# Optimization experiments

Measured on AMD Instinct MI355X. Metric: run time of the kernel, lower is better.

Reference implementation:

```python
import jax, jax.numpy as jnp
import numpy as np

N_P = 2048   # personality nodes
N_W = 89     # word nodes (fixed by user_word_adj[:, :89])
N_ALL = N_P + N_W
B = 16384    # users
E2 = 768     # sentence embedding size
UW = 313     # 89 word cols + 224 extra cols -> 32 + 224 = 256 for share1


def setup_inputs() -> dict:
    key = jax.random.key(0)
    ks = jax.random.split(key, 20)
    rn = lambda k, s, sc=0.1: (jax.random.normal(k, s, jnp.float32) * sc)
    pern_adj = jax.random.randint(ks[2], (N_P, N_P), 0, 2, jnp.int32)
    pern_adj = pern_adj.at[jnp.arange(N_P), jnp.arange(N_P)].set(1)
    word_pern_adj = jax.random.randint(ks[3], (N_ALL, N_ALL), 0, 2, jnp.int32)
    word_pern_adj = word_pern_adj.at[jnp.arange(N_ALL), jnp.arange(N_ALL)].set(1)
    return dict(
        pern_feature=rn(ks[0], (N_P, 256), 1.0),
        word_feature=rn(ks[1], (N_W, 256), 1.0),
        pern_adj=pern_adj,
        word_pern_adj=word_pern_adj,
        user_word_adj=jax.random.uniform(ks[4], (B, UW), jnp.float32),
        sentence_embed=rn(ks[5], (B, E2), 1.0),
        w1=rn(ks[6], (8, 256, 32)), a_src1=rn(ks[7], (8, 32)), a_dst1=rn(ks[8], (8, 32)), bias1=jnp.zeros((32,), jnp.float32),
        w2=rn(ks[9], (8, 256, 32)), a_src2=rn(ks[10], (8, 32)), a_dst2=rn(ks[11], (8, 32)), bias2=jnp.zeros((32,), jnp.float32),
        W_s1=rn(ks[12], (256, 128)), b_s1=jnp.zeros((128,), jnp.float32),
        W_s2=rn(ks[13], (E2, 128)), b_s2=jnp.zeros((128,), jnp.float32),
        W_f1=rn(ks[14], (128, 64)), b_f1=jnp.zeros((64,), jnp.float32),
        W_fa=rn(ks[15], (256, 128)), b_fa=jnp.zeros((128,), jnp.float32),
        W_fb=rn(ks[16], (128, 5)), b_fb=jnp.zeros((5,), jnp.float32),
    )


def gat(h, adj, w, a_src, a_dst, bias):
    # h: (n, f_in); w: (H, f_in, f_out); a_src/a_dst: (H, f_out); adj: (n, n) 0/1
    hp = jnp.einsum('nf,hfo->hno', h, w)                      # (H, n, f_out)
    e_src = jnp.einsum('hno,ho->hn', hp, a_src)               # (H, n)
    e_dst = jnp.einsum('hno,ho->hn', hp, a_dst)               # (H, n)
    e = jax.nn.leaky_relu(e_src[:, :, None] + e_dst[:, None, :], 0.2)  # (H, n, n)
    e = jnp.where(adj[None, :, :] > 0, e, jnp.float32(-1e9))
    attn = jax.nn.softmax(e, axis=-1)
    out = jnp.einsum('hnm,hmo->hno', attn, hp) + bias         # (H, n, f_out)
    return out, attn


def reference(pern_feature, word_feature, pern_adj, word_pern_adj,
              user_word_adj, sentence_embed,
              w1, a_src1, a_dst1, bias1, w2, a_src2, a_dst2, bias2,
              W_s1, b_s1, W_s2, b_s2, W_f1, b_f1, W_fa, b_fa, W_fb, b_fb):
    n_p = pern_feature.shape[0]
    # GAT 1 on personality graph
    h1, attn_pp = gat(pern_feature, pern_adj, w1, a_src1, a_dst1, bias1)
    h1 = jax.nn.elu(jnp.transpose(h1, (1, 0, 2)).reshape(n_p, -1))   # (n_p, 256)
    # dropout is identity at eval time
    h1_wp = jnp.concatenate([word_feature, h1], axis=0)               # (n_w+n_p, 256)
    # GAT 2 on word-personality graph, mean over heads
    h2, attn_wp = gat(h1_wp, word_pern_adj, w2, a_src2, a_dst2, bias2)
    h2 = h2.mean(axis=0)                                              # (n_w+n_p, 32)
    h2_word = h2[:word_feature.shape[0], :]                           # (89, 32)
    # user aggregation over word adjacency + row normalization
    x = user_word_adj[:, :N_W] @ h2_word                              # (B, 32)
    x_c = jnp.concatenate([x, user_word_adj[:, N_W:]], axis=1)        # (B, 256)
    x = x_c / x_c.sum(axis=1, keepdims=True)
    # dual heads
    output1 = x @ W_s1 + b_s1
    output2 = sentence_embed @ W_s2 + b_s2
    output1_new = output1 @ W_f1 + b_f1
    output2_new = output2 @ W_f1 + b_f1
    x_temp = jnp.concatenate([output1, output2], axis=1)
    x_temp = jax.nn.relu(x_temp @ W_fa + b_fa) @ W_fb + b_fb
    return (output1_new, output2_new, x_temp, attn_pp, attn_wp, x)
```

## Files before the change

### kernel.cpp

```cpp
#include <hip/hip_runtime.h>
#include <cstdint>
#include <cstddef>

#define N_P 2048
#define N_W 89
#define N_ALLC 2137
#define BQ 16384
#define E2C 768

typedef __attribute__((ext_vector_type(8))) short short8;
typedef __attribute__((ext_vector_type(4))) float float4v;

__device__ __forceinline__ float waveMax(float v){
#pragma unroll
  for (int o = 32; o > 0; o >>= 1) v = fmaxf(v, __shfl_down(v, o, 64));
  return v;
}
__device__ __forceinline__ float waveSum(float v){
#pragma unroll
  for (int o = 32; o > 0; o >>= 1) v += __shfl_down(v, o, 64);
  return v;
}
__device__ __forceinline__ unsigned short f2bf(float f){
  union { float f; unsigned int u; } v; v.f = f;
  unsigned int u = v.u;
  unsigned int r = (u + 0x7FFFu + ((u >> 16) & 1u)) >> 16;
  return (unsigned short)r;
}

__global__ __launch_bounds__(256) void repack_w(const float* __restrict__ w,
                                                float* __restrict__ wrm) {
  int idx = blockIdx.x * 256 + threadIdx.x;
  int f = idx >> 8, c = idx & 255;
  int h = c >> 5, o = c & 31;
  wrm[idx] = w[h * 8192 + f * 32 + o];
}

__global__ __launch_bounds__(256) void repack_wpk(const float* __restrict__ W,
                                                  unsigned short* __restrict__ out,
                                                  int K, int N) {
  int idx = blockIdx.x * 256 + threadIdx.x;
  if (idx >= K * N) return;
  int k = idx / N, n = idx - k * N;
  int kb = k >> 5, q = (k >> 3) & 3, j = k & 7;
  out[((size_t)(kb * 4 + q) * N + n) * 8 + j] = f2bf(W[idx]);
}

__global__ __launch_bounds__(256) void copy_word(const float* __restrict__ wf,
                                                 float* __restrict__ h1wp) {
  int idx = blockIdx.x * 256 + threadIdx.x;
  if (idx < N_W * 256) h1wp[idx] = wf[idx];
}

__global__ __launch_bounds__(256) void gemm_f32(
    const float* __restrict__ A, int lda,
    const float* __restrict__ B, int ldb,
    float* __restrict__ C, int ldc,
    const float* __restrict__ bias,
    int M, int N, int K, int relu)
{
  __shared__ __align__(16) float As[16][68];
  __shared__ __align__(16) float Bs[16][68];
  int t = threadIdx.x;
  int m0 = blockIdx.x * 64, n0 = blockIdx.y * 64;
  int tm = t >> 4, tn = t & 15;
  int ar = t >> 2, ak = (t & 3) * 4;
  int bk = t >> 4, bn = (t & 15) * 4;
  float acc[4][4] = {};
  for (int k0 = 0; k0 < K; k0 += 16) {
    float4 av = {0.f, 0.f, 0.f, 0.f};
    int arow = m0 + ar;
    if (arow < M) av = *(const float4*)(A + (size_t)arow * lda + k0 + ak);
    As[ak][ar] = av.x; As[ak + 1][ar] = av.y; As[ak + 2][ar] = av.z; As[ak + 3][ar] = av.w;
    *(float4*)&Bs[bk][bn] = *(const float4*)(B + (size_t)(k0 + bk) * ldb + n0 + bn);
    __syncthreads();
#pragma unroll
    for (int kk = 0; kk < 16; ++kk) {
      float4 a4 = *(const float4*)&As[kk][tm * 4];
      float4 b4 = *(const float4*)&Bs[kk][tn * 4];
      float a[4] = {a4.x, a4.y, a4.z, a4.w};
      float b[4] = {b4.x, b4.y, b4.z, b4.w};
#pragma unroll
      for (int i = 0; i < 4; ++i)
#pragma unroll
        for (int j = 0; j < 4; ++j) acc[i][j] += a[i] * b[j];
    }
    __syncthreads();
  }
#pragma unroll
  for (int i = 0; i < 4; ++i) {
    int row = m0 + tm * 4 + i;
    if (row < M) {
      float4 v;
      v.x = acc[i][0]; v.y = acc[i][1]; v.z = acc[i][2]; v.w = acc[i][3];
      *(float4*)(C + (size_t)row * ldc + n0 + tn * 4) = v;
    }
  }
}

__global__ __launch_bounds__(256) void gemm_mfma(
    const float* __restrict__ A, int lda,
    const unsigned short* __restrict__ Wpk, int N,
    const float* __restrict__ bias,
    float* __restrict__ C, int ldc,
    int K, int relu)
{
  int t = threadIdx.x;
  int w = t >> 6, lane = t & 63;
  int col = lane & 15, quad = lane >> 4;
  int rowA = blockIdx.x * 64 + w * 16 + col;
  int n0 = blockIdx.y * 64;
  const float* arow = A + (size_t)rowA * lda;
  float4v acc[4];
#pragma unroll
  for (int nt = 0; nt < 4; ++nt) acc[nt] = (float4v){0.f, 0.f, 0.f, 0.f};
  for (int k0 = 0; k0 < K; k0 += 32) {
    const float* ap = arow + k0 + quad * 8;
    float4 f0 = *(const float4*)(ap);
    float4 f1 = *(const float4*)(ap + 4);
    short8 a;
    a[0] = (short)f2bf(f0.x); a[1] = (short)f2bf(f0.y);
    a[2] = (short)f2bf(f0.z); a[3] = (short)f2bf(f0.w);
    a[4] = (short)f2bf(f1.x); a[5] = (short)f2bf(f1.y);
    a[6] = (short)f2bf(f1.z); a[7] = (short)f2bf(f1.w);
    const unsigned short* wb = Wpk + ((size_t)((k0 >> 5) * 4 + quad) * N + n0 + col) * 8;
#pragma unroll
    for (int nt = 0; nt < 4; ++nt) {
      short8 b = *(const short8*)(wb + (size_t)nt * 16 * 8);
      acc[nt] = __builtin_amdgcn_mfma_f32_16x16x32_bf16(a, b, acc[nt], 0, 0, 0);
    }
  }
  int rbase = blockIdx.x * 64 + w * 16 + quad * 4;
#pragma unroll
  for (int nt = 0; nt < 4; ++nt) {
    int c = n0 + nt * 16 + col;
    float bv = bias[c];
#pragma unroll
    for (int r = 0; r < 4; ++r) {
      float v = acc[nt][r] + bv;
      if (relu) v = fmaxf(v, 0.f);
      C[(size_t)(rbase + r) * ldc + c] = v;
    }
  }
}

__global__ __launch_bounds__(256) void esrc_edst(
    const float* __restrict__ hp,
    const float* __restrict__ a_src,
    const float* __restrict__ a_dst,
    float* __restrict__ es, float* __restrict__ ed, int N)
{
  __shared__ float sa[256], sd[256];
  int t = threadIdx.x;
  sa[t] = a_src[t]; sd[t] = a_dst[t];
  __syncthreads();
  int idx = blockIdx.x * 256 + t;
  if (idx >= N * 8) return;
  int n = idx >> 3, h = idx & 7;
  const float* hpp = hp + (size_t)n * 256 + h * 32;
  const float* ap = sa + h * 32;
  const float* dp = sd + h * 32;
  float s = 0.f, d = 0.f;
#pragma unroll
  for (int o = 0; o < 32; ++o) { float v = hpp[o]; s += v * ap[o]; d += v * dp[o]; }
  es[h * N + n] = s; ed[h * N + n] = d;
}

__global__ __launch_bounds__(256) void attn_softmax(
    const float* __restrict__ es, const float* __restrict__ ed,
    const int* __restrict__ adj,
    float* __restrict__ attn,
    int N)
{
  int h = blockIdx.x, n = blockIdx.y;
  int t = threadIdx.x, lane = t & 63, wid = t >> 6;
  __shared__ float red[4];
  float esv = es[h * N + n];
  const float* edh = ed + (size_t)h * N;
  const int* arow = adj + (size_t)n * N;
  float v[9];
  float lmax = -3e38f;
#pragma unroll
  for (int i = 0; i < 9; ++i) {
    int m = i * 256 + t;
    float x = -3e38f;
    if (m < N) {
      float e = esv + edh[m];
      e = (e >= 0.f) ? e : 0.2f * e;
      x = (arow[m] > 0) ? e : -1e9f;
    }
    v[i] = x; lmax = fmaxf(lmax, x);
  }
  lmax = waveMax(lmax);
  if (lane == 0) red[wid] = lmax;
  __syncthreads();
  float gmax = fmaxf(fmaxf(red[0], red[1]), fmaxf(red[2], red[3]));
  __syncthreads();
  float lsum = 0.f;
#pragma unroll
  for (int i = 0; i < 9; ++i) {
    int m = i * 256 + t;
    if (m < N) { float p = __expf(v[i] - gmax); v[i] = p; lsum += p; }
  }
  lsum = waveSum(lsum);
  if (lane == 0) red[wid] = lsum;
  __syncthreads();
  float inv = 1.f / (red[0] + red[1] + red[2] + red[3]);
  float* out = attn + ((size_t)h * N + n) * N;
#pragma unroll
  for (int i = 0; i < 9; ++i) {
    int m = i * 256 + t;
    if (m < N) out[m] = v[i] * inv;
  }
}

__global__ __launch_bounds__(256) void pv1_partial(
    const float* __restrict__ attn,
    const float* __restrict__ hp,
    float* __restrict__ parts)
{
  __shared__ __align__(16) float As[128][68];
  __shared__ __align__(16) float Bs[64][36];
  int t = threadIdx.x;
  int m0 = blockIdx.x * 128;
  int h  = blockIdx.y;
  int ks = blockIdx.z;
  int ro = t >> 3;
  int co = t & 7;
  float acc[4][4] = {};
  const float* abase = attn + ((size_t)h * N_P + m0) * N_P;
  for (int k0 = ks * 512; k0 < ks * 512 + 512; k0 += 64) {
#pragma unroll
    for (int i = 0; i < 8; ++i) {
      int idx = t + i * 256;
      int r = idx >> 4, c4 = idx & 15;
      float4 v = *(const float4*)(abase + (size_t)r * N_P + k0 + c4 * 4);
      *(float4*)&As[r][c4 * 4] = v;
    }
#pragma unroll
    for (int i = 0; i < 2; ++i) {
      int idx = t + i * 256;
      int r = idx >> 3, c4 = idx & 7;
      float4 v = *(const float4*)(hp + (size_t)(k0 + r) * 256 + h * 32 + c4 * 4);
      *(float4*)&Bs[r][c4 * 4] = v;
    }
    __syncthreads();
#pragma unroll 16
    for (int kk = 0; kk < 64; ++kk) {
      float4 b4 = *(const float4*)&Bs[kk][co * 4];
#pragma unroll
      for (int i = 0; i < 4; ++i) {
        float a = As[ro * 4 + i][kk];
        acc[i][0] += a * b4.x; acc[i][1] += a * b4.y;
        acc[i][2] += a * b4.z; acc[i][3] += a * b4.w;
      }
    }
    __syncthreads();
  }
  float* p = parts + (size_t)ks * (N_P * 256);
#pragma unroll
  for (int i = 0; i < 4; ++i) {
    int row = m0 + ro * 4 + i;
    float4 v; v.x = acc[i][0]; v.y = acc[i][1]; v.z = acc[i][2]; v.w = acc[i][3];
    *(float4*)&p[(size_t)row * 256 + h * 32 + co * 4] = v;
  }
}

__global__ __launch_bounds__(256) void pv1_epilogue(
    const float* __restrict__ parts,
    const float* __restrict__ bias,
    float* __restrict__ h1wp)
{
  int idx = blockIdx.x * 256 + threadIdx.x;
  float s = parts[idx] + parts[idx + N_P * 256] + parts[idx + 2 * N_P * 256] + parts[idx + 3 * N_P * 256];
  s += bias[idx & 31];
  h1wp[(size_t)N_W * 256 + idx] = (s > 0.f) ? s : expm1f(s);
}

__global__ __launch_bounds__(256) void h2w_init(const float* __restrict__ bias,
                                                float* __restrict__ h2w) {
  int idx = blockIdx.x * 256 + threadIdx.x;
  if (idx < N_W * 32) h2w[idx] = bias[idx & 31];
}

__global__ __launch_bounds__(256) void pv2(
    const float* __restrict__ attn,
    const float* __restrict__ hp,
    float* __restrict__ h2w)
{
  int n = blockIdx.x, h = blockIdx.y;
  int t = threadIdx.x, g = t >> 5, o = t & 31;
  const float* arow = attn + ((size_t)h * N_ALLC + n) * N_ALLC;
  float acc = 0.f;
  for (int m = g; m < N_ALLC; m += 8) acc += arow[m] * hp[(size_t)m * 256 + h * 32 + o];
  __shared__ float pv[8][33];
  pv[g][o] = acc;
  __syncthreads();
  if (t < 32) {
    float s = 0.f;
#pragma unroll
    for (int gg = 0; gg < 8; ++gg) s += pv[gg][t];
    atomicAdd(&h2w[n * 32 + t], s * 0.125f);
  }
}

__global__ __launch_bounds__(256) void xnorm_kernel(
    const float* __restrict__ uwa,
    const float* __restrict__ h2w,
    float* __restrict__ xout)
{
  __shared__ float urow[4][320];
  __shared__ float xh[4][33];
  __shared__ float inv[4];
  int t = threadIdx.x;
  int b0 = blockIdx.x * 4;
  for (int idx = t; idx < 4 * 313; idx += 256) {
    int r = idx / 313, j = idx - r * 313;
    urow[r][j] = uwa[(size_t)(b0 + r) * 313 + j];
  }
  __syncthreads();
  if (t < 128) {
    int r = t >> 5, o = t & 31;
    float s = 0.f;
    for (int i = 0; i < N_W; ++i) s += urow[r][i] * h2w[i * 32 + o];
    xh[r][o] = s;
  }
  __syncthreads();
  int lane = t & 63, w = t >> 6;
  float ls = 0.f;
  for (int c = lane; c < 256; c += 64) {
    float v = (c < 32) ? xh[w][c] : urow[w][89 + c - 32];
    ls += v;
  }
  ls = waveSum(ls);
  if (lane == 0) inv[w] = 1.f / ls;
  __syncthreads();
  for (int idx = t; idx < 1024; idx += 256) {
    int r = idx >> 8, c = idx & 255;
    float v = (c < 32) ? xh[r][c] : urow[r][89 + c - 32];
    xout[(size_t)(b0 + r) * 256 + c] = v * inv[r];
  }
}

__global__ __launch_bounds__(256) void final5(
    const float* __restrict__ tb,
    const float* __restrict__ Wfb,
    const float* __restrict__ bfb,
    float* __restrict__ out)
{
  __shared__ float tt[32][129];
  __shared__ float wfb[5][128];
  int t = threadIdx.x;
  int b0 = blockIdx.x * 32;
  for (int idx = t; idx < 32 * 128; idx += 256) {
    int r = idx >> 7, c = idx & 127;
    tt[r][c] = tb[(size_t)(b0 + r) * 128 + c];
  }
  for (int idx = t; idx < 640; idx += 256) {
    int q = idx >> 7, j = idx & 127;
    wfb[q][j] = Wfb[j * 5 + q];
  }
  __syncthreads();
  if (t < 160) {
    int q = t >> 5, r = t & 31;
    float s = bfb[q];
    const float* wq = wfb[q];
    for (int j = 0; j < 128; ++j) s += tt[r][j] * wq[j];
    out[(size_t)(b0 + r) * 5 + q] = s;
  }
}

extern "C" void kernel_launch(void* const* d_in, const int* in_sizes, int n_in,
                              void* d_out, int out_size, void* d_ws, size_t ws_size,
                              hipStream_t stream)
{
  const float* pf   = (const float*)d_in[0];
  const float* wf   = (const float*)d_in[1];
  const int*   adj1 = (const int*)d_in[2];
  const int*   adj2 = (const int*)d_in[3];
  const float* uwa  = (const float*)d_in[4];
  const float* sent = (const float*)d_in[5];
  const float* w1   = (const float*)d_in[6];
  const float* as1  = (const float*)d_in[7];
  const float* ad1  = (const float*)d_in[8];
  const float* b1   = (const float*)d_in[9];
  const float* w2   = (const float*)d_in[10];
  const float* as2  = (const float*)d_in[11];
  const float* ad2  = (const float*)d_in[12];
  const float* b2   = (const float*)d_in[13];
  const float* Ws1  = (const float*)d_in[14];
  const float* bs1  = (const float*)d_in[15];
  const float* Ws2  = (const float*)d_in[16];
  const float* bs2  = (const float*)d_in[17];
  const float* Wf1  = (const float*)d_in[18];
  const float* bf1  = (const float*)d_in[19];
  const float* Wfa  = (const float*)d_in[20];
  const float* bfa  = (const float*)d_in[21];
  const float* Wfb  = (const float*)d_in[22];
  const float* bfb  = (const float*)d_in[23];

  float* ws = (float*)d_ws;
  float* wrm1 = ws;
  float* wrm2 = wrm1 + 65536;
  float* hp1  = wrm2 + 65536;
  float* hp2  = hp1 + (size_t)N_P * 256;
  float* es1v = hp2 + (size_t)N_ALLC * 256;
  float* ed1v = es1v + 8 * N_P;
  float* es2v = ed1v + 8 * N_P;
  float* ed2v = es2v + 8 * N_ALLC;
  float* h1wp = ed2v + 8 * N_ALLC;
  float* h2w  = h1wp + (size_t)N_ALLC * 256;
  float* o12  = h2w + N_W * 32;
  float* tbuf = o12 + (size_t)BQ * 256;
  float* parts = tbuf + (size_t)BQ * 128;
  unsigned short* ws1pk = (unsigned short*)(parts + (size_t)4 * N_P * 256);
  unsigned short* ws2pk = ws1pk + 256 * 128;
  unsigned short* wf1pk = ws2pk + 768 * 128;
  unsigned short* wfapk = wf1pk + 128 * 64;

  float* out = (float*)d_out;
  float* out_o1n = out;
  float* out_o2n = out + (size_t)BQ * 64;
  float* out_xt  = out + (size_t)BQ * 128;
  float* out_app = out_xt + (size_t)BQ * 5;
  float* out_awp = out_app + (size_t)8 * N_P * N_P;
  float* out_x   = out_awp + (size_t)8 * N_ALLC * N_ALLC;

  repack_w<<<256, 256, 0, stream>>>(w1, wrm1);
  repack_w<<<256, 256, 0, stream>>>(w2, wrm2);
  repack_wpk<<<(256 * 128 + 255) / 256, 256, 0, stream>>>(Ws1, ws1pk, 256, 128);
  repack_wpk<<<(768 * 128 + 255) / 256, 256, 0, stream>>>(Ws2, ws2pk, 768, 128);
  repack_wpk<<<(128 * 64 + 255) / 256, 256, 0, stream>>>(Wf1, wf1pk, 128, 64);
  repack_wpk<<<(256 * 128 + 255) / 256, 256, 0, stream>>>(Wfa, wfapk, 256, 128);
  copy_word<<<89, 256, 0, stream>>>(wf, h1wp);

  gemm_f32<<<dim3(32, 4), 256, 0, stream>>>(pf, 256, wrm1, 256, hp1, 256, nullptr, N_P, 256, 256, 0);
  esrc_edst<<<(N_P * 8 + 255) / 256, 256, 0, stream>>>(hp1, as1, ad1, es1v, ed1v, N_P);
  attn_softmax<<<dim3(8, N_P), 256, 0, stream>>>(es1v, ed1v, adj1, out_app, N_P);
  pv1_partial<<<dim3(16, 8, 4), 256, 0, stream>>>(out_app, hp1, parts);
  pv1_epilogue<<<N_P, 256, 0, stream>>>(parts, b1, h1wp);

  gemm_f32<<<dim3(34, 4), 256, 0, stream>>>(h1wp, 256, wrm2, 256, hp2, 256, nullptr, N_ALLC, 256, 256, 0);
  esrc_edst<<<(N_ALLC * 8 + 255) / 256, 256, 0, stream>>>(hp2, as2, ad2, es2v, ed2v, N_ALLC);
  attn_softmax<<<dim3(8, N_ALLC), 256, 0, stream>>>(es2v, ed2v, adj2, out_awp, N_ALLC);

  h2w_init<<<(N_W * 32 + 255) / 256, 256, 0, stream>>>(b2, h2w);
  pv2<<<dim3(N_W, 8), 256, 0, stream>>>(out_awp, hp2, h2w);

  xnorm_kernel<<<BQ / 4, 256, 0, stream>>>(uwa, h2w, out_x);

  gemm_mfma<<<dim3(BQ / 64, 2), 256, 0, stream>>>(out_x, 256, ws1pk, 128, bs1, o12, 256, 256, 0);
  gemm_mfma<<<dim3(BQ / 64, 2), 256, 0, stream>>>(sent, E2C, ws2pk, 128, bs2, o12 + 128, 256, E2C, 0);
  gemm_mfma<<<dim3(BQ / 64, 1), 256, 0, stream>>>(o12, 256, wf1pk, 64, bf1, out_o1n, 64, 128, 0);
  gemm_mfma<<<dim3(BQ / 64, 1), 256, 0, stream>>>(o12 + 128, 256, wf1pk, 64, bf1, out_o2n, 64, 128, 0);
  gemm_mfma<<<dim3(BQ / 64, 2), 256, 0, stream>>>(o12, 256, wfapk, 128, bfa, tbuf, 128, 256, 1);
  final5<<<BQ / 32, 256, 0, stream>>>(tbuf, Wfb, bfb, out_xt);
}
```

Measured before the change: 757.3 us.

## Fuse repacks, move PV1 to bf16 MFMA, fuse dual-head and tail GEMMs

```diff
diff --git a/kernel.cpp b/kernel.cpp
--- a/kernel.cpp
+++ b/kernel.cpp
@@ -27,37 +27,64 @@
   unsigned int r = (u + 0x7FFFu + ((u >> 16) & 1u)) >> 16;
   return (unsigned short)r;
 }
-
-__global__ __launch_bounds__(256) void repack_w(const float* __restrict__ w,
-                                                float* __restrict__ wrm) {
-  int idx = blockIdx.x * 256 + threadIdx.x;
-  int f = idx >> 8, c = idx & 255;
-  int h = c >> 5, o = c & 31;
-  wrm[idx] = w[h * 8192 + f * 32 + o];
-}
-
-__global__ __launch_bounds__(256) void repack_wpk(const float* __restrict__ W,
-                                                  unsigned short* __restrict__ out,
-                                                  int K, int N) {
-  int idx = blockIdx.x * 256 + threadIdx.x;
+__device__ __forceinline__ short8 cvt8(const float* p){
+  float4 f0 = *(const float4*)p;
+  float4 f1 = *(const float4*)(p + 4);
+  short8 a;
+  a[0] = (short)f2bf(f0.x); a[1] = (short)f2bf(f0.y);
+  a[2] = (short)f2bf(f0.z); a[3] = (short)f2bf(f0.w);
+  a[4] = (short)f2bf(f1.x); a[5] = (short)f2bf(f1.y);
+  a[6] = (short)f2bf(f1.z); a[7] = (short)f2bf(f1.w);
+  return a;
+}
+
+__device__ __forceinline__ void wpk_one(const float* __restrict__ W,
+                                        unsigned short* __restrict__ out,
+                                        int K, int N, int idx){
   if (idx >= K * N) return;
   int k = idx / N, n = idx - k * N;
-  int kb = k >> 5, q = (k >> 3) & 3, j = k & 7;
-  out[((size_t)(kb * 4 + q) * N + n) * 8 + j] = f2bf(W[idx]);
-}
-
-__global__ __launch_bounds__(256) void copy_word(const float* __restrict__ wf,
-                                                 float* __restrict__ h1wp) {
-  int idx = blockIdx.x * 256 + threadIdx.x;
-  if (idx < N_W * 256) h1wp[idx] = wf[idx];
+  out[((size_t)((k >> 5) * 4 + ((k >> 3) & 3)) * N + n) * 8 + (k & 7)] = f2bf(W[idx]);
+}
+
+__global__ __launch_bounds__(256) void repack_all(
+    const float* __restrict__ w1, float* __restrict__ wrm1,
+    const float* __restrict__ w2, float* __restrict__ wrm2,
+    const float* __restrict__ Ws1, unsigned short* __restrict__ ws1pk,
+    const float* __restrict__ Ws2, unsigned short* __restrict__ ws2pk,
+    const float* __restrict__ Wf1, unsigned short* __restrict__ wf1pk,
+    const float* __restrict__ Wfa, unsigned short* __restrict__ wfapk,
+    const float* __restrict__ wf, float* __restrict__ h1wp)
+{
+  int b = blockIdx.x, t = threadIdx.x;
+  if (b < 256) {
+    int idx = b * 256 + t;
+    int f = idx >> 8, c = idx & 255;
+    int h = c >> 5, o = c & 31;
+    wrm1[idx] = w1[h * 8192 + f * 32 + o];
+  } else if (b < 512) {
+    int idx = (b - 256) * 256 + t;
+    int f = idx >> 8, c = idx & 255;
+    int h = c >> 5, o = c & 31;
+    wrm2[idx] = w2[h * 8192 + f * 32 + o];
+  } else if (b < 640) {
+    wpk_one(Ws1, ws1pk, 256, 128, (b - 512) * 256 + t);
+  } else if (b < 1024) {
+    wpk_one(Ws2, ws2pk, 768, 128, (b - 640) * 256 + t);
+  } else if (b < 1056) {
+    wpk_one(Wf1, wf1pk, 128, 64, (b - 1024) * 256 + t);
+  } else if (b < 1184) {
+    wpk_one(Wfa, wfapk, 256, 128, (b - 1056) * 256 + t);
+  } else {
+    int idx = (b - 1184) * 256 + t;
+    if (idx < N_W * 256) h1wp[idx] = wf[idx];
+  }
 }
 
 __global__ __launch_bounds__(256) void gemm_f32(
     const float* __restrict__ A, int lda,
     const float* __restrict__ B, int ldb,
     float* __restrict__ C, int ldc,
-    const float* __restrict__ bias,
-    int M, int N, int K, int relu)
+    int M, int N, int K)
 {
   __shared__ __align__(16) float As[16][68];
   __shared__ __align__(16) float Bs[16][68];
@@ -98,72 +125,37 @@
   }
 }
 
-__global__ __launch_bounds__(256) void gemm_mfma(
-    const float* __restrict__ A, int lda,
-    const unsigned short* __restrict__ Wpk, int N,
-    const float* __restrict__ bias,
-    float* __restrict__ C, int ldc,
-    int K, int relu)
-{
-  int t = threadIdx.x;
-  int w = t >> 6, lane = t & 63;
-  int col = lane & 15, quad = lane >> 4;
-  int rowA = blockIdx.x * 64 + w * 16 + col;
-  int n0 = blockIdx.y * 64;
-  const float* arow = A + (size_t)rowA * lda;
-  float4v acc[4];
-#pragma unroll
-  for (int nt = 0; nt < 4; ++nt) acc[nt] = (float4v){0.f, 0.f, 0.f, 0.f};
-  for (int k0 = 0; k0 < K; k0 += 32) {
-    const float* ap = arow + k0 + quad * 8;
-    float4 f0 = *(const float4*)(ap);
-    float4 f1 = *(const float4*)(ap + 4);
-    short8 a;
-    a[0] = (short)f2bf(f0.x); a[1] = (short)f2bf(f0.y);
-    a[2] = (short)f2bf(f0.z); a[3] = (short)f2bf(f0.w);
-    a[4] = (short)f2bf(f1.x); a[5] = (short)f2bf(f1.y);
-    a[6] = (short)f2bf(f1.z); a[7] = (short)f2bf(f1.w);
-    const unsigned short* wb = Wpk + ((size_t)((k0 >> 5) * 4 + quad) * N + n0 + col) * 8;
-#pragma unroll
-    for (int nt = 0; nt < 4; ++nt) {
-      short8 b = *(const short8*)(wb + (size_t)nt * 16 * 8);
-      acc[nt] = __builtin_amdgcn_mfma_f32_16x16x32_bf16(a, b, acc[nt], 0, 0, 0);
-    }
-  }
-  int rbase = blockIdx.x * 64 + w * 16 + quad * 4;
-#pragma unroll
-  for (int nt = 0; nt < 4; ++nt) {
-    int c = n0 + nt * 16 + col;
-    float bv = bias[c];
-#pragma unroll
-    for (int r = 0; r < 4; ++r) {
-      float v = acc[nt][r] + bv;
-      if (relu) v = fmaxf(v, 0.f);
-      C[(size_t)(rbase + r) * ldc + c] = v;
-    }
-  }
-}
-
 __global__ __launch_bounds__(256) void esrc_edst(
     const float* __restrict__ hp,
     const float* __restrict__ a_src,
     const float* __restrict__ a_dst,
-    float* __restrict__ es, float* __restrict__ ed, int N)
+    float* __restrict__ es, float* __restrict__ ed,
+    unsigned short* __restrict__ hppk,
+    float* __restrict__ h2w, const float* __restrict__ b2,
+    int N, int do_pack)
 {
   __shared__ float sa[256], sd[256];
   int t = threadIdx.x;
   sa[t] = a_src[t]; sd[t] = a_dst[t];
   __syncthreads();
   int idx = blockIdx.x * 256 + t;
+  if (h2w != nullptr && idx < N_W * 32) h2w[idx] = b2[idx & 31];
   if (idx >= N * 8) return;
   int n = idx >> 3, h = idx & 7;
   const float* hpp = hp + (size_t)n * 256 + h * 32;
   const float* ap = sa + h * 32;
   const float* dp = sd + h * 32;
   float s = 0.f, d = 0.f;
-#pragma unroll
-  for (int o = 0; o < 32; ++o) { float v = hpp[o]; s += v * ap[o]; d += v * dp[o]; }
+  float hv[32];
+#pragma unroll
+  for (int o = 0; o < 32; ++o) { hv[o] = hpp[o]; s += hv[o] * ap[o]; d += hv[o] * dp[o]; }
   es[h * N + n] = s; ed[h * N + n] = d;
+  if (do_pack) {
+    unsigned short* dst = hppk + (size_t)h * (N_P * 32)
+                        + (size_t)((n >> 5) * 4 + ((n >> 3) & 3)) * 256 + (n & 7);
+#pragma unroll
+    for (int o = 0; o < 32; ++o) dst[o * 8] = f2bf(hv[o]);
+  }
 }
 
 __global__ __launch_bounds__(256) void attn_softmax(
@@ -214,73 +206,51 @@
   }
 }
 
-__global__ __launch_bounds__(256) void pv1_partial(
+__global__ __launch_bounds__(256) void pv1_mfma(
     const float* __restrict__ attn,
-    const float* __restrict__ hp,
-    float* __restrict__ parts)
-{
-  __shared__ __align__(16) float As[128][68];
-  __shared__ __align__(16) float Bs[64][36];
-  int t = threadIdx.x;
-  int m0 = blockIdx.x * 128;
-  int h  = blockIdx.y;
-  int ks = blockIdx.z;
-  int ro = t >> 3;
-  int co = t & 7;
-  float acc[4][4] = {};
-  const float* abase = attn + ((size_t)h * N_P + m0) * N_P;
-  for (int k0 = ks * 512; k0 < ks * 512 + 512; k0 += 64) {
-#pragma unroll
-    for (int i = 0; i < 8; ++i) {
-      int idx = t + i * 256;
-      int r = idx >> 4, c4 = idx & 15;
-      float4 v = *(const float4*)(abase + (size_t)r * N_P + k0 + c4 * 4);
-      *(float4*)&As[r][c4 * 4] = v;
-    }
-#pragma unroll
-    for (int i = 0; i < 2; ++i) {
-      int idx = t + i * 256;
-      int r = idx >> 3, c4 = idx & 7;
-      float4 v = *(const float4*)(hp + (size_t)(k0 + r) * 256 + h * 32 + c4 * 4);
-      *(float4*)&Bs[r][c4 * 4] = v;
-    }
-    __syncthreads();
-#pragma unroll 16
-    for (int kk = 0; kk < 64; ++kk) {
-      float4 b4 = *(const float4*)&Bs[kk][co * 4];
-#pragma unroll
-      for (int i = 0; i < 4; ++i) {
-        float a = As[ro * 4 + i][kk];
-        acc[i][0] += a * b4.x; acc[i][1] += a * b4.y;
-        acc[i][2] += a * b4.z; acc[i][3] += a * b4.w;
-      }
-    }
-    __syncthreads();
-  }
-  float* p = parts + (size_t)ks * (N_P * 256);
-#pragma unroll
-  for (int i = 0; i < 4; ++i) {
-    int row = m0 + ro * 4 + i;
-    float4 v; v.x = acc[i][0]; v.y = acc[i][1]; v.z = acc[i][2]; v.w = acc[i][3];
-    *(float4*)&p[(size_t)row * 256 + h * 32 + co * 4] = v;
-  }
-}
-
-__global__ __launch_bounds__(256) void pv1_epilogue(
-    const float* __restrict__ parts,
+    const unsigned short* __restrict__ hppk,
     const float* __restrict__ bias,
     float* __restrict__ h1wp)
 {
-  int idx = blockIdx.x * 256 + threadIdx.x;
-  float s = parts[idx] + parts[idx + N_P * 256] + parts[idx + 2 * N_P * 256] + parts[idx + 3 * N_P * 256];
-  s += bias[idx & 31];
-  h1wp[(size_t)N_W * 256 + idx] = (s > 0.f) ? s : expm1f(s);
-}
-
-__global__ __launch_bounds__(256) void h2w_init(const float* __restrict__ bias,
-                                                float* __restrict__ h2w) {
-  int idx = blockIdx.x * 256 + threadIdx.x;
-  if (idx < N_W * 32) h2w[idx] = bias[idx & 31];
+  __shared__ float red[2][16][33];
+  int t = threadIdx.x, w = t >> 6, lane = t & 63;
+  int col = lane & 15, quad = lane >> 4;
+  int kh = w >> 1, rh = (w & 1) * 16;
+  int h = blockIdx.y;
+  int row0 = blockIdx.x * 32;
+  int rowA = row0 + rh + col;
+  const float* arow = attn + ((size_t)h * N_P + rowA) * N_P + kh * 1024;
+  const unsigned short* wb0 = hppk + (size_t)h * (N_P * 32) + (size_t)kh * 32768;
+  float4v acc0 = {0.f, 0.f, 0.f, 0.f}, acc1 = {0.f, 0.f, 0.f, 0.f};
+#pragma unroll 4
+  for (int kk = 0; kk < 1024; kk += 32) {
+    short8 a = cvt8(arow + kk + quad * 8);
+    const unsigned short* wb = wb0 + ((size_t)((kk >> 5) * 4 + quad) * 32 + col) * 8;
+    short8 b0 = *(const short8*)(wb);
+    short8 b1 = *(const short8*)(wb + 128);
+    acc0 = __builtin_amdgcn_mfma_f32_16x16x32_bf16(a, b0, acc0, 0, 0, 0);
+    acc1 = __builtin_amdgcn_mfma_f32_16x16x32_bf16(a, b1, acc1, 0, 0, 0);
+  }
+  if (kh == 1) {
+#pragma unroll
+    for (int r = 0; r < 4; ++r) {
+      red[w & 1][quad * 4 + r][col] = acc0[r];
+      red[w & 1][quad * 4 + r][16 + col] = acc1[r];
+    }
+  }
+  __syncthreads();
+  if (kh == 0) {
+    int rbase = row0 + rh + quad * 4;
+#pragma unroll
+    for (int r = 0; r < 4; ++r) {
+      float v0 = acc0[r] + red[w & 1][quad * 4 + r][col] + bias[col];
+      float v1 = acc1[r] + red[w & 1][quad * 4 + r][16 + col] + bias[16 + col];
+      v0 = (v0 > 0.f) ? v0 : expm1f(v0);
+      v1 = (v1 > 0.f) ? v1 : expm1f(v1);
+      float* dst = h1wp + (size_t)(N_W + rbase + r) * 256 + h * 32;
+      dst[col] = v0; dst[16 + col] = v1;
+    }
+  }
 }
 
 __global__ __launch_bounds__(256) void pv2(
@@ -342,31 +312,128 @@
   }
 }
 
-__global__ __launch_bounds__(256) void final5(
-    const float* __restrict__ tb,
+__global__ __launch_bounds__(256) void o12_fused(
+    const float* __restrict__ x,
+    const float* __restrict__ sent,
+    const unsigned short* __restrict__ ws1pk,
+    const unsigned short* __restrict__ ws2pk,
+    const float* __restrict__ bs1,
+    const float* __restrict__ bs2,
+    unsigned short* __restrict__ o12bf)
+{
+  int t = threadIdx.x, w = t >> 6, lane = t & 63;
+  int col = lane & 15, quad = lane >> 4;
+  int rowA = blockIdx.x * 64 + w * 16 + col;
+  int half = blockIdx.y;
+  const float* A = half ? (sent + (size_t)rowA * E2C) : (x + (size_t)rowA * 256);
+  const unsigned short* wpk = half ? ws2pk : ws1pk;
+  const float* bias = half ? bs2 : bs1;
+  int K = half ? E2C : 256;
+  float4v acc[8];
+#pragma unroll
+  for (int i = 0; i < 8; ++i) acc[i] = (float4v){0.f, 0.f, 0.f, 0.f};
+#pragma unroll 4
+  for (int k0 = 0; k0 < K; k0 += 32) {
+    short8 a = cvt8(A + k0 + quad * 8);
+    const unsigned short* wb = wpk + ((size_t)((k0 >> 5) * 4 + quad) * 128 + col) * 8;
+#pragma unroll
+    for (int nt = 0; nt < 8; ++nt)
+      acc[nt] = __builtin_amdgcn_mfma_f32_16x16x32_bf16(a, *(const short8*)(wb + nt * 128), acc[nt], 0, 0, 0);
+  }
+  int rbase = blockIdx.x * 64 + w * 16 + quad * 4;
+  int cb = half * 128;
+#pragma unroll
+  for (int nt = 0; nt < 8; ++nt) {
+    int c = nt * 16 + col;
+    float bv = bias[c];
+#pragma unroll
+    for (int r = 0; r < 4; ++r)
+      o12bf[(size_t)(rbase + r) * 256 + cb + c] = f2bf(acc[nt][r] + bv);
+  }
+}
+
+__global__ __launch_bounds__(256) void tail_fused(
+    const unsigned short* __restrict__ o12bf,
+    const unsigned short* __restrict__ wf1pk,
+    const unsigned short* __restrict__ wfapk,
+    const float* __restrict__ bf1,
+    const float* __restrict__ bfa,
     const float* __restrict__ Wfb,
     const float* __restrict__ bfb,
-    float* __restrict__ out)
-{
-  __shared__ float tt[32][129];
-  __shared__ float wfb[5][128];
+    float* __restrict__ o1n, float* __restrict__ o2n, float* __restrict__ xt)
+{
+  __shared__ float sWfb[640];
   int t = threadIdx.x;
-  int b0 = blockIdx.x * 32;
-  for (int idx = t; idx < 32 * 128; idx += 256) {
-    int r = idx >> 7, c = idx & 127;
-    tt[r][c] = tb[(size_t)(b0 + r) * 128 + c];
-  }
-  for (int idx = t; idx < 640; idx += 256) {
-    int q = idx >> 7, j = idx & 127;
-    wfb[q][j] = Wfb[j * 5 + q];
-  }
-  __syncthreads();
-  if (t < 160) {
-    int q = t >> 5, r = t & 31;
-    float s = bfb[q];
-    const float* wq = wfb[q];
-    for (int j = 0; j < 128; ++j) s += tt[r][j] * wq[j];
-    out[(size_t)(b0 + r) * 5 + q] = s;
+  for (int i = t; i < 640; i += 256) sWfb[i] = Wfb[i];
+  __syncthreads();
+  int w = t >> 6, lane = t & 63;
+  int col = lane & 15, quad = lane >> 4;
+  int rowA = blockIdx.x * 64 + w * 16 + col;
+  const unsigned short* ar = o12bf + (size_t)rowA * 256;
+  float4v aT[8], a1[4], a2[4];
+#pragma unroll
+  for (int i = 0; i < 8; ++i) aT[i] = (float4v){0.f, 0.f, 0.f, 0.f};
+#pragma unroll
+  for (int i = 0; i < 4; ++i) { a1[i] = (float4v){0.f, 0.f, 0.f, 0.f}; a2[i] = (float4v){0.f, 0.f, 0.f, 0.f}; }
+#pragma unroll
+  for (int k0 = 0; k0 < 128; k0 += 32) {
+    short8 a = *(const short8*)(ar + k0 + quad * 8);
+    const unsigned short* wbT = wfapk + ((size_t)((k0 >> 5) * 4 + quad) * 128 + col) * 8;
+    const unsigned short* wb1 = wf1pk + ((size_t)((k0 >> 5) * 4 + quad) * 64 + col) * 8;
+#pragma unroll
+    for (int nt = 0; nt < 8; ++nt)
+      aT[nt] = __builtin_amdgcn_mfma_f32_16x16x32_bf16(a, *(const short8*)(wbT + nt * 128), aT[nt], 0, 0, 0);
+#pragma unroll
+    for (int nt = 0; nt < 4; ++nt)
+      a1[nt] = __builtin_amdgcn_mfma_f32_16x16x32_bf16(a, *(const short8*)(wb1 + nt * 128), a1[nt], 0, 0, 0);
+  }
+#pragma unroll
+  for (int k0 = 128; k0 < 256; k0 += 32) {
+    short8 a = *(const short8*)(ar + k0 + quad * 8);
+    const unsigned short* wbT = wfapk + ((size_t)((k0 >> 5) * 4 + quad) * 128 + col) * 8;
+    const unsigned short* wb1 = wf1pk + ((size_t)(((k0 - 128) >> 5) * 4 + quad) * 64 + col) * 8;
+#pragma unroll
+    for (int nt = 0; nt < 8; ++nt)
+      aT[nt] = __builtin_amdgcn_mfma_f32_16x16x32_bf16(a, *(const short8*)(wbT + nt * 128), aT[nt], 0, 0, 0);
+#pragma unroll
+    for (int nt = 0; nt < 4; ++nt)
+      a2[nt] = __builtin_amdgcn_mfma_f32_16x16x32_bf16(a, *(const short8*)(wb1 + nt * 128), a2[nt], 0, 0, 0);
+  }
+  int rbase = blockIdx.x * 64 + w * 16 + quad * 4;
+#pragma unroll
+  for (int nt = 0; nt < 4; ++nt) {
+    int c = nt * 16 + col;
+    float b1v = bf1[c];
+#pragma unroll
+    for (int r = 0; r < 4; ++r) {
+      o1n[(size_t)(rbase + r) * 64 + c] = a1[nt][r] + b1v;
+      o2n[(size_t)(rbase + r) * 64 + c] = a2[nt][r] + b1v;
+    }
+  }
+  float xp[4][5] = {};
+#pragma unroll
+  for (int nt = 0; nt < 8; ++nt) {
+    int c = nt * 16 + col;
+    float bav = bfa[c];
+#pragma unroll
+    for (int r = 0; r < 4; ++r) {
+      float tv = fmaxf(aT[nt][r] + bav, 0.f);
+#pragma unroll
+      for (int q = 0; q < 5; ++q) xp[r][q] += tv * sWfb[c * 5 + q];
+    }
+  }
+#pragma unroll
+  for (int m = 1; m <= 8; m <<= 1) {
+#pragma unroll
+    for (int r = 0; r < 4; ++r)
+#pragma unroll
+      for (int q = 0; q < 5; ++q) xp[r][q] += __shfl_xor(xp[r][q], m, 64);
+  }
+  if (col == 0) {
+#pragma unroll
+    for (int r = 0; r < 4; ++r)
+#pragma unroll
+      for (int q = 0; q < 5; ++q) xt[(size_t)(rbase + r) * 5 + q] = xp[r][q] + bfb[q];
   }
 }
 
@@ -407,13 +474,12 @@
   float* es1v = hp2 + (size_t)N_ALLC * 256;
   float* ed1v = es1v + 8 * N_P;
   float* es2v = ed1v + 8 * N_P;
-  float* ed2v = es2v + 8 * N_ALLC;
-  float* h1wp = ed2v + 8 * N_ALLC;
+  float* ed2v = es2v + 17152;
+  float* h1wp = ed2v + 17152;
   float* h2w  = h1wp + (size_t)N_ALLC * 256;
-  float* o12  = h2w + N_W * 32;
-  float* tbuf = o12 + (size_t)BQ * 256;
-  float* parts = tbuf + (size_t)BQ * 128;
-  unsigned short* ws1pk = (unsigned short*)(parts + (size_t)4 * N_P * 256);
+  unsigned short* o12bf = (unsigned short*)(h2w + 2880);
+  unsigned short* hp1pk = o12bf + (size_t)BQ * 256;
+  unsigned short* ws1pk = hp1pk + 8 * N_P * 32;
   unsigned short* ws2pk = ws1pk + 256 * 128;
   unsigned short* wf1pk = ws2pk + 768 * 128;
   unsigned short* wfapk = wf1pk + 128 * 64;
@@ -426,33 +492,20 @@
   float* out_awp = out_app + (size_t)8 * N_P * N_P;
   float* out_x   = out_awp + (size_t)8 * N_ALLC * N_ALLC;
 
-  repack_w<<<256, 256, 0, stream>>>(w1, wrm1);
-  repack_w<<<256, 256, 0, stream>>>(w2, wrm2);
-  repack_wpk<<<(256 * 128 + 255) / 256, 256, 0, stream>>>(Ws1, ws1pk, 256, 128);
-  repack_wpk<<<(768 * 128 + 255) / 256, 256, 0, stream>>>(Ws2, ws2pk, 768, 128);
-  repack_wpk<<<(128 * 64 + 255) / 256, 256, 0, stream>>>(Wf1, wf1pk, 128, 64);
-  repack_wpk<<<(256 * 128 + 255) / 256, 256, 0, stream>>>(Wfa, wfapk, 256, 128);
-  copy_word<<<89, 256, 0, stream>>>(wf, h1wp);
-
-  gemm_f32<<<dim3(32, 4), 256, 0, stream>>>(pf, 256, wrm1, 256, hp1, 256, nullptr, N_P, 256, 256, 0);
-  esrc_edst<<<(N_P * 8 + 255) / 256, 256, 0, stream>>>(hp1, as1, ad1, es1v, ed1v, N_P);
+  repack_all<<<1273, 256, 0, stream>>>(w1, wrm1, w2, wrm2, Ws1, ws1pk, Ws2, ws2pk,
+                                       Wf1, wf1pk, Wfa, wfapk, wf, h1wp);
+  gemm_f32<<<dim3(32, 4), 256, 0, stream>>>(pf, 256, wrm1, 256, hp1, 256, N_P, 256, 256);
+  esrc_edst<<<(N_P * 8 + 255) / 256, 256, 0, stream>>>(hp1, as1, ad1, es1v, ed1v,
+                                                       hp1pk, nullptr, nullptr, N_P, 1);
   attn_softmax<<<dim3(8, N_P), 256, 0, stream>>>(es1v, ed1v, adj1, out_app, N_P);
-  pv1_partial<<<dim3(16, 8, 4), 256, 0, stream>>>(out_app, hp1, parts);
-  pv1_epilogue<<<N_P, 256, 0, stream>>>(parts, b1, h1wp);
-
-  gemm_f32<<<dim3(34, 4), 256, 0, stream>>>(h1wp, 256, wrm2, 256, hp2, 256, nullptr, N_ALLC, 256, 256, 0);
-  esrc_edst<<<(N_ALLC * 8 + 255) / 256, 256, 0, stream>>>(hp2, as2, ad2, es2v, ed2v, N_ALLC);
+  pv1_mfma<<<dim3(64, 8), 256, 0, stream>>>(out_app, hp1pk, b1, h1wp);
+  gemm_f32<<<dim3(34, 4), 256, 0, stream>>>(h1wp, 256, wrm2, 256, hp2, 256, N_ALLC, 256, 256);
+  esrc_edst<<<(N_ALLC * 8 + 255) / 256, 256, 0, stream>>>(hp2, as2, ad2, es2v, ed2v,
+                                                          nullptr, h2w, b2, N_ALLC, 0);
   attn_softmax<<<dim3(8, N_ALLC), 256, 0, stream>>>(es2v, ed2v, adj2, out_awp, N_ALLC);
-
-  h2w_init<<<(N_W * 32 + 255) / 256, 256, 0, stream>>>(b2, h2w);
   pv2<<<dim3(N_W, 8), 256, 0, stream>>>(out_awp, hp2, h2w);
-
   xnorm_kernel<<<BQ / 4, 256, 0, stream>>>(uwa, h2w, out_x);
-
-  gemm_mfma<<<dim3(BQ / 64, 2), 256, 0, stream>>>(out_x, 256, ws1pk, 128, bs1, o12, 256, 256, 0);
-  gemm_mfma<<<dim3(BQ / 64, 2), 256, 0, stream>>>(sent, E2C, ws2pk, 128, bs2, o12 + 128, 256, E2C, 0);
-  gemm_mfma<<<dim3(BQ / 64, 1), 256, 0, stream>>>(o12, 256, wf1pk, 64, bf1, out_o1n, 64, 128, 0);
-  gemm_mfma<<<dim3(BQ / 64, 1), 256, 0, stream>>>(o12 + 128, 256, wf1pk, 64, bf1, out_o2n, 64, 128, 0);
-  gemm_mfma<<<dim3(BQ / 64, 2), 256, 0, stream>>>(o12, 256, wfapk, 128, bfa, tbuf, 128, 256, 1);
-  final5<<<BQ / 32, 256, 0, stream>>>(tbuf, Wfb, bfb, out_xt);
-}
+  o12_fused<<<dim3(BQ / 64, 2), 256, 0, stream>>>(out_x, sent, ws1pk, ws2pk, bs1, bs2, o12bf);
+  tail_fused<<<BQ / 64, 256, 0, stream>>>(o12bf, wf1pk, wfapk, bf1, bfa, Wfb, bfb,
+                                          out_o1n, out_o2n, out_xt);
+}
```

Result: faster. 707.9 us (-6.5%).
